# Optimization experiments

Hardware: AMD Instinct MI355X
Metric: run time of the kernel (lower is better)

Reference implementation:

```python
import jax, jax.numpy as jnp
import numpy as np

# RReLU in eval mode == leaky relu with slope (lower+upper)/2
_SLOPE = (0.001 + 0.004) / 2.0  # 0.0025

def _rrelu(x):
    return jnp.where(x >= 0, x, _SLOPE * x)

_DIMS = [(8, 8), (8, 4), (4, 4), (4, 4), (4, 4), (4, 4), (4, 1),
         (1, 4), (4, 4), (4, 4), (4, 4), (4, 4), (4, 8)]
_NAMES = ['in', 'h1', 'h2', 'h3', 'h4', 'h5', 'encode',
          'h6', 'h7', 'h8', 'h9', 'h10', 'decode']


def setup_inputs() -> dict:
    key = jax.random.key(0)
    keys = jax.random.split(key, 1 + 2 * len(_DIMS))
    inp = {'x_in': jax.random.normal(keys[0], (4194304, 8), dtype=jnp.float32)}
    for i, (name, (fi, fo)) in enumerate(zip(_NAMES, _DIMS)):
        bound = 1.0 / np.sqrt(fi)
        inp[f'W_{name}'] = jax.random.uniform(keys[1 + 2 * i], (fi, fo),
                                              minval=-bound, maxval=bound,
                                              dtype=jnp.float32)
        inp[f'b_{name}'] = jax.random.uniform(keys[2 + 2 * i], (fo,),
                                              minval=-bound, maxval=bound,
                                              dtype=jnp.float32)
    return inp


def reference(x_in, W_in, b_in, W_h1, b_h1, W_h2, b_h2, W_h3, b_h3,
              W_h4, b_h4, W_h5, b_h5, W_encode, b_encode, W_h6, b_h6,
              W_h7, b_h7, W_h8, b_h8, W_h9, b_h9, W_h10, b_h10,
              W_decode, b_decode):
    lin = lambda x, W, b: x @ W + b
    x = x_in  # (x - mean)/std with mean=0, std=1 is identity
    x = lin(_rrelu(lin(x, W_in, b_in)), W_h1, b_h1)
    x = x + lin(_rrelu(lin(x, W_h2, b_h2)), W_h3, b_h3)
    x = x + lin(_rrelu(lin(x, W_h4, b_h4)), W_h5, b_h5)
    x_encode = _rrelu(lin(x, W_encode, b_encode))
    x = _rrelu(lin(x_encode, W_h6, b_h6))
    x = x + lin(_rrelu(lin(x, W_h7, b_h7)), W_h8, b_h8)
    x = x + lin(_rrelu(lin(x, W_h9, b_h9)), W_h10, b_h10)
    x_decode = _rrelu(lin(x, W_decode, b_decode))
    return (x_encode, x_decode)
```

## Files before the change

kernel.cpp:

```cpp
#include <hip/hip_runtime.h>

#define N_ROWS 4194304
#define RPT 4
#define BLOCK 256

__device__ __forceinline__ float rrelu(float v) {
    return v >= 0.0f ? v : 0.0025f * v;
}

struct Weights {
    const float *W_in,  *b_in,  *W_h1,  *b_h1,  *W_h2, *b_h2, *W_h3, *b_h3,
                *W_h4,  *b_h4,  *W_h5,  *b_h5,  *W_enc, *b_enc,
                *W_h6,  *b_h6,  *W_h7,  *b_h7,  *W_h8, *b_h8, *W_h9, *b_h9,
                *W_h10, *b_h10, *W_dec, *b_dec;
};

__device__ __forceinline__ void resblock(float x[RPT][4],
                                         const float* __restrict__ Wa,
                                         const float* __restrict__ ba,
                                         const float* __restrict__ Wb,
                                         const float* __restrict__ bb) {
    float t[RPT][4];
#pragma unroll
    for (int j = 0; j < 4; ++j) {
#pragma unroll
        for (int k = 0; k < RPT; ++k) {
            float acc = ba[j];
#pragma unroll
            for (int i = 0; i < 4; ++i) acc = fmaf(x[k][i], Wa[i * 4 + j], acc);
            t[k][j] = rrelu(acc);
        }
    }
#pragma unroll
    for (int j = 0; j < 4; ++j) {
#pragma unroll
        for (int k = 0; k < RPT; ++k) {
            float acc = bb[j];
#pragma unroll
            for (int i = 0; i < 4; ++i) acc = fmaf(t[k][i], Wb[i * 4 + j], acc);
            x[k][j] += acc;
        }
    }
}

__global__ __launch_bounds__(BLOCK) void ann_fused_kernel(
    const float* __restrict__ x_in, float* __restrict__ out, Weights w) {
    const int tid = blockIdx.x * BLOCK + threadIdx.x;
    const int T = N_ROWS / RPT;

    float xin[RPT][8];
#pragma unroll
    for (int k = 0; k < RPT; ++k) {
        const float4* p =
            reinterpret_cast<const float4*>(x_in + (size_t)(tid + k * T) * 8);
        float4 a = p[0], b = p[1];
        xin[k][0] = a.x; xin[k][1] = a.y; xin[k][2] = a.z; xin[k][3] = a.w;
        xin[k][4] = b.x; xin[k][5] = b.y; xin[k][6] = b.z; xin[k][7] = b.w;
    }

    float t8[RPT][8];
#pragma unroll
    for (int j = 0; j < 8; ++j) {
#pragma unroll
        for (int k = 0; k < RPT; ++k) {
            float acc = w.b_in[j];
#pragma unroll
            for (int i = 0; i < 8; ++i) acc = fmaf(xin[k][i], w.W_in[i * 8 + j], acc);
            t8[k][j] = rrelu(acc);
        }
    }

    float x[RPT][4];
#pragma unroll
    for (int j = 0; j < 4; ++j) {
#pragma unroll
        for (int k = 0; k < RPT; ++k) {
            float acc = w.b_h1[j];
#pragma unroll
            for (int i = 0; i < 8; ++i) acc = fmaf(t8[k][i], w.W_h1[i * 4 + j], acc);
            x[k][j] = acc;
        }
    }

    resblock(x, w.W_h2, w.b_h2, w.W_h3, w.b_h3);
    resblock(x, w.W_h4, w.b_h4, w.W_h5, w.b_h5);

    float e[RPT];
#pragma unroll
    for (int k = 0; k < RPT; ++k) {
        float acc = w.b_enc[0];
#pragma unroll
        for (int i = 0; i < 4; ++i) acc = fmaf(x[k][i], w.W_enc[i], acc);
        e[k] = rrelu(acc);
    }

#pragma unroll
    for (int j = 0; j < 4; ++j) {
#pragma unroll
        for (int k = 0; k < RPT; ++k) {
            x[k][j] = rrelu(fmaf(e[k], w.W_h6[j], w.b_h6[j]));
        }
    }

    resblock(x, w.W_h7, w.b_h7, w.W_h8, w.b_h8);
    resblock(x, w.W_h9, w.b_h9, w.W_h10, w.b_h10);

    float d[RPT][8];
#pragma unroll
    for (int j = 0; j < 8; ++j) {
#pragma unroll
        for (int k = 0; k < RPT; ++k) {
            float acc = w.b_dec[j];
#pragma unroll
            for (int i = 0; i < 4; ++i) acc = fmaf(x[k][i], w.W_dec[i * 8 + j], acc);
            d[k][j] = rrelu(acc);
        }
    }

#pragma unroll
    for (int k = 0; k < RPT; ++k) {
        const int row = tid + k * T;
        out[row] = e[k];
        float4* q = reinterpret_cast<float4*>(out + N_ROWS + (size_t)row * 8);
        q[0] = make_float4(d[k][0], d[k][1], d[k][2], d[k][3]);
        q[1] = make_float4(d[k][4], d[k][5], d[k][6], d[k][7]);
    }
}

extern "C" void kernel_launch(void* const* d_in, const int* in_sizes, int n_in,
                              void* d_out, int out_size, void* d_ws, size_t ws_size,
                              hipStream_t stream) {
    const float* x_in = (const float*)d_in[0];
    Weights w;
    w.W_in  = (const float*)d_in[1];  w.b_in  = (const float*)d_in[2];
    w.W_h1  = (const float*)d_in[3];  w.b_h1  = (const float*)d_in[4];
    w.W_h2  = (const float*)d_in[5];  w.b_h2  = (const float*)d_in[6];
    w.W_h3  = (const float*)d_in[7];  w.b_h3  = (const float*)d_in[8];
    w.W_h4  = (const float*)d_in[9];  w.b_h4  = (const float*)d_in[10];
    w.W_h5  = (const float*)d_in[11]; w.b_h5  = (const float*)d_in[12];
    w.W_enc = (const float*)d_in[13]; w.b_enc = (const float*)d_in[14];
    w.W_h6  = (const float*)d_in[15]; w.b_h6  = (const float*)d_in[16];
    w.W_h7  = (const float*)d_in[17]; w.b_h7  = (const float*)d_in[18];
    w.W_h8  = (const float*)d_in[19]; w.b_h8  = (const float*)d_in[20];
    w.W_h9  = (const float*)d_in[21]; w.b_h9  = (const float*)d_in[22];
    w.W_h10 = (const float*)d_in[23]; w.b_h10 = (const float*)d_in[24];
    w.W_dec = (const float*)d_in[25]; w.b_dec = (const float*)d_in[26];
    float* out = (float*)d_out;

    const int total_threads = N_ROWS / RPT;
    dim3 grid(total_threads / BLOCK), block(BLOCK);
    ann_fused_kernel<<<grid, block, 0, stream>>>(x_in, out, w);
}
```

Baseline: 303.6 us.

## Process rows sequentially per thread with software-prefetched next row

Restructures the kernel so each thread handles 8 rows in a non-unrolled loop, computing one row at a time and prefetching the next row's input while computing the current one. The aim is to cut register pressure from the interleaved multi-row arrays so occupancy rises, while still overlapping loads with compute. It also rewrites rrelu as fmaxf(v, slope*v) to avoid a compare/select. Risk: the serial per-row dependency chain loses the ILP that interleaving gave, and the grid is halved.

```diff
diff --git a/kernel.cpp b/kernel.cpp
--- a/kernel.cpp
+++ b/kernel.cpp
@@ -1,11 +1,11 @@
 #include <hip/hip_runtime.h>
 
 #define N_ROWS 4194304
-#define RPT 4
+#define RPT 8
 #define BLOCK 256
 
 __device__ __forceinline__ float rrelu(float v) {
-    return v >= 0.0f ? v : 0.0025f * v;
+    return fmaxf(v, 0.0025f * v);
 }
 
 struct Weights {
@@ -15,31 +15,63 @@
                 *W_h10, *b_h10, *W_dec, *b_dec;
 };
 
-__device__ __forceinline__ void resblock(float x[RPT][4],
+__device__ __forceinline__ void resblock(float x[4],
                                          const float* __restrict__ Wa,
                                          const float* __restrict__ ba,
                                          const float* __restrict__ Wb,
                                          const float* __restrict__ bb) {
-    float t[RPT][4];
+    float t[4];
 #pragma unroll
     for (int j = 0; j < 4; ++j) {
+        float acc = ba[j];
 #pragma unroll
-        for (int k = 0; k < RPT; ++k) {
-            float acc = ba[j];
-#pragma unroll
-            for (int i = 0; i < 4; ++i) acc = fmaf(x[k][i], Wa[i * 4 + j], acc);
-            t[k][j] = rrelu(acc);
-        }
+        for (int i = 0; i < 4; ++i) acc = fmaf(x[i], Wa[i * 4 + j], acc);
+        t[j] = rrelu(acc);
     }
 #pragma unroll
     for (int j = 0; j < 4; ++j) {
+        float acc = bb[j];
 #pragma unroll
-        for (int k = 0; k < RPT; ++k) {
-            float acc = bb[j];
+        for (int i = 0; i < 4; ++i) acc = fmaf(t[i], Wb[i * 4 + j], acc);
+        x[j] += acc;
+    }
+}
+
+__device__ __forceinline__ void net_row(const float xin[8], const Weights& w,
+                                        float& e_out, float d[8]) {
+    float t8[8];
 #pragma unroll
-            for (int i = 0; i < 4; ++i) acc = fmaf(t[k][i], Wb[i * 4 + j], acc);
-            x[k][j] += acc;
-        }
+    for (int j = 0; j < 8; ++j) {
+        float acc = w.b_in[j];
+#pragma unroll
+        for (int i = 0; i < 8; ++i) acc = fmaf(xin[i], w.W_in[i * 8 + j], acc);
+        t8[j] = rrelu(acc);
+    }
+    float x[4];
+#pragma unroll
+    for (int j = 0; j < 4; ++j) {
+        float acc = w.b_h1[j];
+#pragma unroll
+        for (int i = 0; i < 8; ++i) acc = fmaf(t8[i], w.W_h1[i * 4 + j], acc);
+        x[j] = acc;
+    }
+    resblock(x, w.W_h2, w.b_h2, w.W_h3, w.b_h3);
+    resblock(x, w.W_h4, w.b_h4, w.W_h5, w.b_h5);
+    float e = w.b_enc[0];
+#pragma unroll
+    for (int i = 0; i < 4; ++i) e = fmaf(x[i], w.W_enc[i], e);
+    e = rrelu(e);
+    e_out = e;
+#pragma unroll
+    for (int j = 0; j < 4; ++j) x[j] = rrelu(fmaf(e, w.W_h6[j], w.b_h6[j]));
+    resblock(x, w.W_h7, w.b_h7, w.W_h8, w.b_h8);
+    resblock(x, w.W_h9, w.b_h9, w.W_h10, w.b_h10);
+#pragma unroll
+    for (int j = 0; j < 8; ++j) {
+        float acc = w.b_dec[j];
+#pragma unroll
+        for (int i = 0; i < 4; ++i) acc = fmaf(x[i], w.W_dec[i * 8 + j], acc);
+        d[j] = rrelu(acc);
     }
 }
 
@@ -48,82 +80,28 @@
     const int tid = blockIdx.x * BLOCK + threadIdx.x;
     const int T = N_ROWS / RPT;
 
-    float xin[RPT][8];
-#pragma unroll
+    const float4* p0 = reinterpret_cast<const float4*>(x_in) + (size_t)tid * 2;
+    float4 a_next = p0[0];
+    float4 b_next = p0[1];
+
+#pragma unroll 1
     for (int k = 0; k < RPT; ++k) {
-        const float4* p =
-            reinterpret_cast<const float4*>(x_in + (size_t)(tid + k * T) * 8);
-        float4 a = p[0], b = p[1];
-        xin[k][0] = a.x; xin[k][1] = a.y; xin[k][2] = a.z; xin[k][3] = a.w;
-        xin[k][4] = b.x; xin[k][5] = b.y; xin[k][6] = b.z; xin[k][7] = b.w;
-    }
+        float4 a = a_next, b = b_next;
+        if (k + 1 < RPT) {
+            const float4* pn = reinterpret_cast<const float4*>(x_in) +
+                               ((size_t)tid + (size_t)(k + 1) * T) * 2;
+            a_next = pn[0];
+            b_next = pn[1];
+        }
+        float xin[8] = {a.x, a.y, a.z, a.w, b.x, b.y, b.z, b.w};
+        float e, d[8];
+        net_row(xin, w, e, d);
 
-    float t8[RPT][8];
-#pragma unroll
-    for (int j = 0; j < 8; ++j) {
-#pragma unroll
-        for (int k = 0; k < RPT; ++k) {
-            float acc = w.b_in[j];
-#pragma unroll
-            for (int i = 0; i < 8; ++i) acc = fmaf(xin[k][i], w.W_in[i * 8 + j], acc);
-            t8[k][j] = rrelu(acc);
-        }
-    }
-
-    float x[RPT][4];
-#pragma unroll
-    for (int j = 0; j < 4; ++j) {
-#pragma unroll
-        for (int k = 0; k < RPT; ++k) {
-            float acc = w.b_h1[j];
-#pragma unroll
-            for (int i = 0; i < 8; ++i) acc = fmaf(t8[k][i], w.W_h1[i * 4 + j], acc);
-            x[k][j] = acc;
-        }
-    }
-
-    resblock(x, w.W_h2, w.b_h2, w.W_h3, w.b_h3);
-    resblock(x, w.W_h4, w.b_h4, w.W_h5, w.b_h5);
-
-    float e[RPT];
-#pragma unroll
-    for (int k = 0; k < RPT; ++k) {
-        float acc = w.b_enc[0];
-#pragma unroll
-        for (int i = 0; i < 4; ++i) acc = fmaf(x[k][i], w.W_enc[i], acc);
-        e[k] = rrelu(acc);
-    }
-
-#pragma unroll
-    for (int j = 0; j < 4; ++j) {
-#pragma unroll
-        for (int k = 0; k < RPT; ++k) {
-            x[k][j] = rrelu(fmaf(e[k], w.W_h6[j], w.b_h6[j]));
-        }
-    }
-
-    resblock(x, w.W_h7, w.b_h7, w.W_h8, w.b_h8);
-    resblock(x, w.W_h9, w.b_h9, w.W_h10, w.b_h10);
-
-    float d[RPT][8];
-#pragma unroll
-    for (int j = 0; j < 8; ++j) {
-#pragma unroll
-        for (int k = 0; k < RPT; ++k) {
-            float acc = w.b_dec[j];
-#pragma unroll
-            for (int i = 0; i < 4; ++i) acc = fmaf(x[k][i], w.W_dec[i * 8 + j], acc);
-            d[k][j] = rrelu(acc);
-        }
-    }
-
-#pragma unroll
-    for (int k = 0; k < RPT; ++k) {
         const int row = tid + k * T;
-        out[row] = e[k];
+        out[row] = e;
         float4* q = reinterpret_cast<float4*>(out + N_ROWS + (size_t)row * 8);
-        q[0] = make_float4(d[k][0], d[k][1], d[k][2], d[k][3]);
-        q[1] = make_float4(d[k][4], d[k][5], d[k][6], d[k][7]);
+        q[0] = make_float4(d[0], d[1], d[2], d[3]);
+        q[1] = make_float4(d[4], d[5], d[6], d[7]);
     }
 }
 
```

Result: slower. 314.4 us (+3.6%).
